# Optimization experiments

Measured on AMD Instinct MI355X. Metric: run time of the kernel, lower is better.

## Reference

```python
import jax, jax.numpy as jnp
import numpy as np

K = 512
H = 8

def setup_inputs() -> dict:
    key = jax.random.key(0)
    ks = jax.random.split(key, 6)
    b, t, k = 4, 2048, K
    scale = 1.0 / np.sqrt(k)
    return {
        "x": jax.random.normal(ks[0], (b, t, k), dtype=jnp.float32),
        "Wq": jax.random.normal(ks[1], (k, k), dtype=jnp.float32) * scale,
        "Wk": jax.random.normal(ks[2], (k, k), dtype=jnp.float32) * scale,
        "Wv": jax.random.normal(ks[3], (k, k), dtype=jnp.float32) * scale,
        "Wo": jax.random.normal(ks[4], (k, k), dtype=jnp.float32) * scale,
        "bo": jax.random.normal(ks[5], (k,), dtype=jnp.float32) * 0.01,
    }

def reference(x, Wq, Wk, Wv, Wo, bo):
    b, t, k = x.shape
    h = H
    s = k // h
    # nn.Linear: y = x @ W.T ; weights stored [out, in]
    q = (x @ Wq.T).reshape(b, t, h, s)
    kk = (x @ Wk.T).reshape(b, t, h, s)
    v = (x @ Wv.T).reshape(b, t, h, s)
    # scores: note original divides by sqrt(k) (full model dim), not sqrt(s)
    dot = jnp.einsum("bqhs,bkhs->bhqk", q, kk) / jnp.sqrt(jnp.float32(k))
    attn = jax.nn.softmax(dot, axis=-1)
    out = jnp.einsum("bhqk,bkhs->bqhs", attn, v).reshape(b, t, k)
    return out @ Wo.T + bo
```

## Files before the change

kernel.cpp:

```cpp
#include <hip/hip_runtime.h>

typedef _Float16 f16;
typedef _Float16 f16x8 __attribute__((ext_vector_type(8)));
typedef _Float16 f16x4 __attribute__((ext_vector_type(4)));
typedef float    f32x4 __attribute__((ext_vector_type(4)));
typedef __fp16   fp16x2 __attribute__((ext_vector_type(2)));

#define MFMA(a,b,c) __builtin_amdgcn_mfma_f32_16x16x32_f16((a),(b),(c),0,0,0)

#if __has_builtin(__builtin_amdgcn_exp2f)
#define EXP2(x) __builtin_amdgcn_exp2f(x)
#else
#define EXP2(x) exp2f(x)
#endif

__device__ __forceinline__ void gl_lds16(const void* g, void* l) {
  __builtin_amdgcn_global_load_lds(
      (__attribute__((address_space(1))) void*)(void*)(g),
      (__attribute__((address_space(3))) void*)(l),
      16, 0, 0);
}

__device__ __forceinline__ int SWZ(int row) {
  return ((row & 3) | ((row >> 1) & 4)) << 4;
}

__global__ __launch_bounds__(256) void k_convert(
    const float* __restrict__ x, const float* __restrict__ Wq,
    const float* __restrict__ Wk, const float* __restrict__ Wv,
    const float* __restrict__ Wo,
    f16* __restrict__ x_h, f16* __restrict__ wqkv_h, f16* __restrict__ wo_h) {
  const int XQ    = (8192 * 512) / 4;
  const int WQKVQ = (1536 * 512) / 4;
  const int WOQ   = (512 * 512) / 4;
  const int total = XQ + WQKVQ + WOQ;
  for (int q = blockIdx.x * blockDim.x + threadIdx.x; q < total;
       q += gridDim.x * blockDim.x) {
    const float* src;
    f16* dst;
    if (q < XQ) {
      src = x + q * 4;
      dst = x_h + q * 4;
    } else if (q < XQ + WQKVQ) {
      int j  = q - XQ;
      int r  = j >> 7;
      int c0 = (j & 127) * 4;
      const float* w = (r < 512) ? Wq : (r < 1024) ? Wk : Wv;
      src = w + (r & 511) * 512 + c0;
      dst = wqkv_h + j * 4;
    } else {
      int j = q - XQ - WQKVQ;
      src = Wo + j * 4;
      dst = wo_h + j * 4;
    }
    float4 v = *(const float4*)src;
    f16x4 o = {(f16)v.x, (f16)v.y, (f16)v.z, (f16)v.w};
    *(f16x4*)dst = o;
  }
}

__device__ __forceinline__ void gemm_core(const f16* __restrict__ A,
                                          const f16* __restrict__ B,
                                          int bm, int bn, f32x4 (&acc)[4][4],
                                          char* smem) {
  f16* As = (f16*)smem;
  f16* Bs = (f16*)(smem + 32768);
  const int tid  = threadIdx.x;
  const int lane = tid & 63;
  const int w    = tid >> 6;
  const int wr   = (w >> 1) & 1, wc = w & 1;
  const int r0   = tid >> 3;
  const int cb   = (tid & 7) << 4;

  auto stage = [&](int buf, int kt) {
#pragma unroll
    for (int inst = 0; inst < 4; ++inst) {
      const int row  = inst * 32 + r0;
      const int csrc = cb ^ ((row & 7) << 4);
      gl_lds16(A + (bm + row) * 512 + kt + (csrc >> 1),
               (char*)As + buf * 16384 + inst * 4096 + w * 1024);
      gl_lds16(B + (bn + row) * 512 + kt + (csrc >> 1),
               (char*)Bs + buf * 16384 + inst * 4096 + w * 1024);
    }
  };

  stage(0, 0);
#pragma unroll
  for (int t = 0; t < 8; ++t) {
    const int cur = t & 1;
    asm volatile("s_waitcnt vmcnt(0)" ::: "memory");
    __builtin_amdgcn_s_barrier();
    __builtin_amdgcn_sched_barrier(0);
    if (t < 7) stage(cur ^ 1, (t + 1) * 64);
    f16x8 af[4][2], bf[4][2];
#pragma unroll
    for (int i = 0; i < 4; ++i) {
      const int ra = wr * 64 + i * 16 + (lane & 15);
      const int rb = wc * 64 + i * 16 + (lane & 15);
#pragma unroll
      for (int ks = 0; ks < 2; ++ks) {
        const int cc = ks * 64 + ((lane >> 4) << 4);
        af[i][ks] = *(const f16x8*)((const char*)As + cur * 16384 + ra * 128 + (cc ^ ((ra & 7) << 4)));
        bf[i][ks] = *(const f16x8*)((const char*)Bs + cur * 16384 + rb * 128 + (cc ^ ((rb & 7) << 4)));
      }
    }
    __builtin_amdgcn_s_setprio(1);
#pragma unroll
    for (int i = 0; i < 4; ++i)
#pragma unroll
      for (int j = 0; j < 4; ++j) {
        acc[i][j] = MFMA(af[i][0], bf[j][0], acc[i][j]);
        acc[i][j] = MFMA(af[i][1], bf[j][1], acc[i][j]);
      }
    __builtin_amdgcn_s_setprio(0);
  }
}

__global__ __launch_bounds__(256) void k_gemm_qkv(
    const f16* __restrict__ A, const f16* __restrict__ B,
    f16* __restrict__ q_h, f16* __restrict__ k_h, f16* __restrict__ vt_h) {
  __shared__ char smem[65536];
  const int bm = blockIdx.x * 128;
  const int bn = blockIdx.y * 128;
  const bool isV = (bn >= 1024);

  f32x4 acc[4][4] = {};
  if (isV) gemm_core(B, A, bn, bm, acc, smem);
  else     gemm_core(A, B, bm, bn, acc, smem);

  const int tid  = threadIdx.x;
  const int lane = tid & 63;
  const int w    = tid >> 6;
  const int wr   = (w >> 1) & 1, wc = w & 1;
  const float qscale = (bn < 512) ? 0.044194173824159216f * 1.4426950408889634f : 1.0f;

  __syncthreads();
  f16* T = (f16*)smem;
#pragma unroll
  for (int i = 0; i < 4; ++i) {
    const int rr = wr * 64 + i * 16 + ((lane >> 4) << 2);
#pragma unroll
    for (int j = 0; j < 4; ++j) {
      const int cc = wc * 64 + j * 16 + (lane & 15);
#pragma unroll
      for (int r = 0; r < 4; ++r)
        T[(rr + r) * 136 + cc] = (f16)(acc[i][j][r] * qscale);
    }
  }
  __syncthreads();

  f16* dst_qk = (bn < 512) ? q_h : k_h;
#pragma unroll
  for (int k = 0; k < 8; ++k) {
    const int idx  = k * 256 + tid;
    const int row  = idx >> 4;
    const int col8 = (idx & 15) * 8;
    const f16x8 v = *(const f16x8*)(T + row * 136 + col8);
    if (!isV) {
      const int m = bm + row, b = m >> 11, t = m & 2047;
      const int nn = (bn + col8) & 511, h = nn >> 6, s = nn & 63;
      *(f16x8*)(dst_qk + ((size_t)((b * 8 + h) * 2048 + t)) * 64 + s) = v;
    } else {
      const int nn = (bn - 1024) + row, h = nn >> 6, s = nn & 63;
      const int m = bm + col8, b = m >> 11, t = m & 2047;
      *(f16x8*)(vt_h + ((size_t)((b * 8 + h) * 64 + s)) * 2048 + t) = v;
    }
  }
}

__global__ __launch_bounds__(512, 2) void k_attn(
    const f16* __restrict__ q_h, const f16* __restrict__ k_h,
    const f16* __restrict__ vt_h, f16* __restrict__ a_h) {
  __shared__ char smem[65536];

  const int tid  = threadIdx.x;
  const int lane = tid & 63;
  const int w    = tid >> 6;
  const int g    = w >> 2;
  const int wg   = w & 3;

  int id = blockIdx.x;
  id = (id & 7) * 32 + (id >> 3);
  const int qt = (id & 7) * 256;
  const int bh = id >> 3;

  const f16* qb = q_h + (size_t)bh * 2048 * 64;
  const f16* kb = k_h + (size_t)bh * 2048 * 64;
  const f16* vb = vt_h + (size_t)bh * 64 * 2048;

  auto KsP = [&](int grp, int buf) { return smem + grp * 32768 + buf * 16384; };
  auto VsP = [&](int grp, int buf) { return smem + grp * 32768 + buf * 16384 + 8192; };

  const int m  = lane & 15;
  const int hi = lane >> 4;

  f16x8 qf[4][2];
#pragma unroll
  for (int i = 0; i < 4; ++i) {
    const int qrow = qt + wg * 64 + i * 16 + m;
#pragma unroll
    for (int ks = 0; ks < 2; ++ks)
      qf[i][ks] = *(const f16x8*)(qb + qrow * 64 + ks * 32 + hi * 8);
  }

  f32x4 oacc[4][4] = {};
  float lsum[4]    = {0.f, 0.f, 0.f, 0.f};

  const int gt  = tid & 255;
  const int r0  = gt >> 3;
  const int cbb = (tid & 7) << 4;

  auto stage = [&](int buf, int t) {
    const int ktv = g * 1024 + t * 64;
#pragma unroll
    for (int inst = 0; inst < 2; ++inst) {
      const int row  = inst * 32 + r0;
      const int csrc = cbb ^ SWZ(row);
      gl_lds16(kb + (ktv + row) * 64 + (csrc >> 1),
               KsP(g, buf) + inst * 4096 + wg * 1024);
      gl_lds16(vb + row * 2048 + ktv + (csrc >> 1),
               VsP(g, buf) + inst * 4096 + wg * 1024);
    }
  };

  auto pack4 = [](float a, float b, float c, float d) -> unsigned long long {
    union { fp16x2 h2[2]; unsigned long long u; } t;
    t.h2[0] = __builtin_amdgcn_cvt_pkrtz(a, b);
    t.h2[1] = __builtin_amdgcn_cvt_pkrtz(c, d);
    return t.u;
  };

  auto tile = [&](const char* ksb, const char* vsb) {
    f16x8 kf[4][2];
#pragma unroll
    for (int n = 0; n < 4; ++n) {
      const int row = ((n >> 1) << 5) + ((m >> 2) << 3) + ((n & 1) << 2) + (m & 3);
      const int sw  = SWZ(row);
#pragma unroll
      for (int ks = 0; ks < 2; ++ks) {
        const int c = (ks * 64 + (hi << 4)) ^ sw;
        kf[n][ks] = *(const f16x8*)(ksb + row * 128 + c);
      }
    }
    f32x4 sf[4][4];
#pragma unroll
    for (int i = 0; i < 4; ++i)
#pragma unroll
      for (int n = 0; n < 4; ++n) {
        f32x4 s = {0.f, 0.f, 0.f, 0.f};
        s = MFMA(kf[n][0], qf[i][0], s);
        s = MFMA(kf[n][1], qf[i][1], s);
        sf[i][n] = s;
      }
    f16x8 pa[4][2];
#pragma unroll
    for (int i = 0; i < 4; ++i) {
      f32x4 e[4];
#pragma unroll
      for (int n = 0; n < 4; ++n) {
        e[n][0] = EXP2(sf[i][n][0]);
        e[n][1] = EXP2(sf[i][n][1]);
        e[n][2] = EXP2(sf[i][n][2]);
        e[n][3] = EXP2(sf[i][n][3]);
      }
      const f32x4 ssum = (e[0] + e[1]) + (e[2] + e[3]);
      lsum[i] += (ssum[0] + ssum[1]) + (ssum[2] + ssum[3]);
#pragma unroll
      for (int ks = 0; ks < 2; ++ks) {
        union { unsigned long long u[2]; f16x8 v; } u;
        u.u[0] = pack4(e[2 * ks][0], e[2 * ks][1], e[2 * ks][2], e[2 * ks][3]);
        u.u[1] = pack4(e[2 * ks + 1][0], e[2 * ks + 1][1],
                       e[2 * ks + 1][2], e[2 * ks + 1][3]);
        pa[i][ks] = u.v;
      }
    }
#pragma unroll
    for (int n = 0; n < 4; ++n) {
      const int row = n * 16 + m;
      const int sw  = SWZ(row);
      const f16x8 vf0 = *(const f16x8*)(vsb + row * 128 + ((hi << 4) ^ sw));
      const f16x8 vf1 = *(const f16x8*)(vsb + row * 128 + ((64 + (hi << 4)) ^ sw));
#pragma unroll
      for (int i = 0; i < 4; ++i) {
        oacc[i][n] = MFMA(pa[i][0], vf0, oacc[i][n]);
        oacc[i][n] = MFMA(pa[i][1], vf1, oacc[i][n]);
      }
    }
  };

  stage(0, 0);
  for (int j = 0; j < 16; ++j) {
    const int cur = j & 1;
    asm volatile("s_waitcnt vmcnt(0)" ::: "memory");
    __builtin_amdgcn_s_barrier();
    __builtin_amdgcn_sched_barrier(0);
    if (j < 15) stage(cur ^ 1, j + 1);
    tile(KsP(g, cur), VsP(g, cur));
  }

  float lfin[4];
#pragma unroll
  for (int i = 0; i < 4; ++i) {
    float t = lsum[i] + __shfl_xor(lsum[i], 16, 64);
    lfin[i] = t + __shfl_xor(t, 32, 64);
  }

  __syncthreads();
  float* Ol = (float*)smem;
  float* l1 = (float*)(smem + 34816);

  const int b2 = bh >> 3, h2 = bh & 7;
#pragma unroll
  for (int p = 0; p < 2; ++p) {
    if (g == 1 && (wg >> 1) == p) {
#pragma unroll
      for (int i = 0; i < 4; ++i)
#pragma unroll
        for (int r = 0; r < 4; ++r) {
          const int ql = (wg * 64 + i * 16 + hi * 4 + r) & 127;
#pragma unroll
          for (int n = 0; n < 4; ++n)
            Ol[ql * 68 + n * 16 + m] = oacc[i][n][r];
        }
      if (hi == 0)
#pragma unroll
        for (int i = 0; i < 4; ++i)
          l1[(wg * 64 + i * 16 + m) & 127] = lfin[i];
    }
    __syncthreads();
    if (g == 0 && (wg >> 1) == p) {
#pragma unroll
      for (int i = 0; i < 4; ++i) {
        float lself[4];
#pragma unroll
        for (int r = 0; r < 4; ++r)
          lself[r] = __shfl(lfin[i], (hi << 2) + r, 64);
#pragma unroll
        for (int r = 0; r < 4; ++r) {
          const int qg = wg * 64 + i * 16 + hi * 4 + r;
          const int ql = qg & 127;
          const float rl = 1.0f / (lself[r] + l1[ql]);
          const int qrow = qt + qg;
#pragma unroll
          for (int n = 0; n < 4; ++n) {
            const int s = n * 16 + m;
            const float o = oacc[i][n][r] + Ol[ql * 68 + s];
            a_h[(size_t)(b2 * 2048 + qrow) * 512 + h2 * 64 + s] = (f16)(o * rl);
          }
        }
      }
    }
    __syncthreads();
  }
}

__global__ __launch_bounds__(256) void k_gemm_out(
    const f16* __restrict__ A, const f16* __restrict__ B,
    const float* __restrict__ bo, float* __restrict__ out) {
  __shared__ char smem[65536];
  const int bm = blockIdx.x * 128;
  const int bn = blockIdx.y * 128;
  f32x4 acc[4][4] = {};
  gemm_core(A, B, bm, bn, acc, smem);

  const int tid  = threadIdx.x;
  const int lane = tid & 63;
  const int w    = tid >> 6;
  const int wr   = (w >> 1) & 1, wc = w & 1;
#pragma unroll
  for (int i = 0; i < 4; ++i) {
    const int m0 = bm + wr * 64 + i * 16 + ((lane >> 4) << 2);
#pragma unroll
    for (int j = 0; j < 4; ++j) {
      const int n = bn + wc * 64 + j * 16 + (lane & 15);
      const float bias = bo[n];
#pragma unroll
      for (int r = 0; r < 4; ++r)
        out[(size_t)(m0 + r) * 512 + n] = acc[i][j][r] + bias;
    }
  }
}

extern "C" void kernel_launch(void* const* d_in, const int* in_sizes, int n_in,
                              void* d_out, int out_size, void* d_ws, size_t ws_size,
                              hipStream_t stream) {
  const float* x  = (const float*)d_in[0];
  const float* Wq = (const float*)d_in[1];
  const float* Wk = (const float*)d_in[2];
  const float* Wv = (const float*)d_in[3];
  const float* Wo = (const float*)d_in[4];
  const float* bo = (const float*)d_in[5];
  float* out = (float*)d_out;

  char* ws = (char*)d_ws;
  f16* x_h    = (f16*)(ws);
  f16* wqkv_h = (f16*)(ws + 8388608);
  f16* wo_h   = (f16*)(ws + 9961472);
  f16* q_h    = (f16*)(ws + 10485760);
  f16* k_h    = (f16*)(ws + 18874368);
  f16* vt_h   = (f16*)(ws + 27262976);
  f16* a_h    = (f16*)(ws + 35651584);
  (void)ws_size; (void)in_sizes; (void)n_in; (void)out_size;

  k_convert<<<2048, 256, 0, stream>>>(x, Wq, Wk, Wv, Wo, x_h, wqkv_h, wo_h);
  k_gemm_qkv<<<dim3(64, 12), 256, 0, stream>>>(x_h, wqkv_h, q_h, k_h, vt_h);
  k_attn<<<256, 512, 0, stream>>>(q_h, k_h, vt_h, a_h);
  k_gemm_out<<<dim3(64, 4), 256, 0, stream>>>(a_h, wo_h, bo, out);
}
```

Before: 81.82 us.

## Fuse fp32-to-fp16 conversion of x into QKV GEMM loads and remap tiles

Removes the separate x conversion pass. The QKV GEMM now loads fp32 x tiles straight into registers, converts them to fp16 and writes them into swizzled LDS, while weight tiles still go through direct global-to-LDS loads. This saves a full write and re-read of the 8 MB fp16 copy of x. The grid becomes 1D with a tile remapping that groups blocks, likely to improve L2 reuse across XCDs. The cost is register pressure and VALU conversion work inside the GEMM, and every N-tile block that shares the same x rows now converts them again.

```diff
diff --git a/kernel.cpp b/kernel.cpp
--- a/kernel.cpp
+++ b/kernel.cpp
@@ -25,31 +25,25 @@
   return ((row & 3) | ((row >> 1) & 4)) << 4;
 }
 
-__global__ __launch_bounds__(256) void k_convert(
-    const float* __restrict__ x, const float* __restrict__ Wq,
-    const float* __restrict__ Wk, const float* __restrict__ Wv,
-    const float* __restrict__ Wo,
-    f16* __restrict__ x_h, f16* __restrict__ wqkv_h, f16* __restrict__ wo_h) {
-  const int XQ    = (8192 * 512) / 4;
+__global__ __launch_bounds__(256) void k_convert_w(
+    const float* __restrict__ Wq, const float* __restrict__ Wk,
+    const float* __restrict__ Wv, const float* __restrict__ Wo,
+    f16* __restrict__ wqkv_h, f16* __restrict__ wo_h) {
   const int WQKVQ = (1536 * 512) / 4;
   const int WOQ   = (512 * 512) / 4;
-  const int total = XQ + WQKVQ + WOQ;
+  const int total = WQKVQ + WOQ;
   for (int q = blockIdx.x * blockDim.x + threadIdx.x; q < total;
        q += gridDim.x * blockDim.x) {
     const float* src;
     f16* dst;
-    if (q < XQ) {
-      src = x + q * 4;
-      dst = x_h + q * 4;
-    } else if (q < XQ + WQKVQ) {
-      int j  = q - XQ;
-      int r  = j >> 7;
-      int c0 = (j & 127) * 4;
+    if (q < WQKVQ) {
+      int r  = q >> 7;
+      int c0 = (q & 127) * 4;
       const float* w = (r < 512) ? Wq : (r < 1024) ? Wk : Wv;
       src = w + (r & 511) * 512 + c0;
-      dst = wqkv_h + j * 4;
+      dst = wqkv_h + q * 4;
     } else {
-      int j = q - XQ - WQKVQ;
+      int j = q - WQKVQ;
       src = Wo + j * 4;
       dst = wo_h + j * 4;
     }
@@ -116,17 +110,102 @@
   }
 }
 
+template <bool XA>
+__device__ __forceinline__ void gemm_core_fx(const float* __restrict__ X, int bx,
+                                             const f16* __restrict__ W, int bw,
+                                             f32x4 (&acc)[4][4], char* smem) {
+  char* XsB = smem + (XA ? 0 : 32768);
+  char* WsB = smem + (XA ? 32768 : 0);
+  const int tid  = threadIdx.x;
+  const int lane = tid & 63;
+  const int w    = tid >> 6;
+  const int wr   = (w >> 1) & 1, wc = w & 1;
+  const int r0   = tid >> 3;
+  const int cb   = (tid & 7) << 4;
+
+  float4 xr[4][2];
+  auto loadX = [&](int kt) {
+#pragma unroll
+    for (int inst = 0; inst < 4; ++inst) {
+      const int row  = inst * 32 + r0;
+      const int csrc = cb ^ ((row & 7) << 4);
+      const float* src = X + (size_t)(bx + row) * 512 + kt + (csrc >> 1);
+      xr[inst][0] = *(const float4*)src;
+      xr[inst][1] = *(const float4*)(src + 4);
+    }
+  };
+  auto writeX = [&](int buf) {
+#pragma unroll
+    for (int inst = 0; inst < 4; ++inst) {
+      f16x8 h;
+      h[0] = (f16)xr[inst][0].x; h[1] = (f16)xr[inst][0].y;
+      h[2] = (f16)xr[inst][0].z; h[3] = (f16)xr[inst][0].w;
+      h[4] = (f16)xr[inst][1].x; h[5] = (f16)xr[inst][1].y;
+      h[6] = (f16)xr[inst][1].z; h[7] = (f16)xr[inst][1].w;
+      *(f16x8*)(XsB + buf * 16384 + inst * 4096 + tid * 16) = h;
+    }
+  };
+  auto stageW = [&](int buf, int kt) {
+#pragma unroll
+    for (int inst = 0; inst < 4; ++inst) {
+      const int row  = inst * 32 + r0;
+      const int csrc = cb ^ ((row & 7) << 4);
+      gl_lds16(W + (bw + row) * 512 + kt + (csrc >> 1),
+               WsB + buf * 16384 + inst * 4096 + w * 1024);
+    }
+  };
+
+  loadX(0);
+  stageW(0, 0);
+  writeX(0);
+#pragma unroll
+  for (int t = 0; t < 8; ++t) {
+    const int cur = t & 1;
+    asm volatile("s_waitcnt vmcnt(0) lgkmcnt(0)" ::: "memory");
+    __builtin_amdgcn_s_barrier();
+    __builtin_amdgcn_sched_barrier(0);
+    if (t < 7) {
+      loadX((t + 1) * 64);
+      stageW(cur ^ 1, (t + 1) * 64);
+    }
+    f16x8 af[4][2], bf[4][2];
+#pragma unroll
+    for (int i = 0; i < 4; ++i) {
+      const int ra = wr * 64 + i * 16 + (lane & 15);
+      const int rb = wc * 64 + i * 16 + (lane & 15);
+#pragma unroll
+      for (int ks = 0; ks < 2; ++ks) {
+        const int cc = ks * 64 + ((lane >> 4) << 4);
+        af[i][ks] = *(const f16x8*)(smem + cur * 16384 + ra * 128 + (cc ^ ((ra & 7) << 4)));
+        bf[i][ks] = *(const f16x8*)(smem + 32768 + cur * 16384 + rb * 128 + (cc ^ ((rb & 7) << 4)));
+      }
+    }
+    __builtin_amdgcn_s_setprio(1);
+#pragma unroll
+    for (int i = 0; i < 4; ++i)
+#pragma unroll
+      for (int j = 0; j < 4; ++j) {
+        acc[i][j] = MFMA(af[i][0], bf[j][0], acc[i][j]);
+        acc[i][j] = MFMA(af[i][1], bf[j][1], acc[i][j]);
+      }
+    __builtin_amdgcn_s_setprio(0);
+    if (t < 7) writeX(cur ^ 1);
+  }
+}
+
 __global__ __launch_bounds__(256) void k_gemm_qkv(
-    const f16* __restrict__ A, const f16* __restrict__ B,
+    const float* __restrict__ X, const f16* __restrict__ B,
     f16* __restrict__ q_h, f16* __restrict__ k_h, f16* __restrict__ vt_h) {
   __shared__ char smem[65536];
-  const int bm = blockIdx.x * 128;
-  const int bn = blockIdx.y * 128;
+  int wg = blockIdx.x;
+  const int nw  = (wg & 7) * 96 + (wg >> 3);
+  const int bm  = (nw / 12) * 128;
+  const int bn  = (nw % 12) * 128;
   const bool isV = (bn >= 1024);
 
   f32x4 acc[4][4] = {};
-  if (isV) gemm_core(B, A, bn, bm, acc, smem);
-  else     gemm_core(A, B, bm, bn, acc, smem);
+  if (isV) gemm_core_fx<false>(X, bm, B, bn, acc, smem);
+  else     gemm_core_fx<true>(X, bm, B, bn, acc, smem);
 
   const int tid  = threadIdx.x;
   const int lane = tid & 63;
@@ -393,7 +472,6 @@
   float* out = (float*)d_out;
 
   char* ws = (char*)d_ws;
-  f16* x_h    = (f16*)(ws);
   f16* wqkv_h = (f16*)(ws + 8388608);
   f16* wo_h   = (f16*)(ws + 9961472);
   f16* q_h    = (f16*)(ws + 10485760);
@@ -402,8 +480,8 @@
   f16* a_h    = (f16*)(ws + 35651584);
   (void)ws_size; (void)in_sizes; (void)n_in; (void)out_size;
 
-  k_convert<<<2048, 256, 0, stream>>>(x, Wq, Wk, Wv, Wo, x_h, wqkv_h, wo_h);
-  k_gemm_qkv<<<dim3(64, 12), 256, 0, stream>>>(x_h, wqkv_h, q_h, k_h, vt_h);
+  k_convert_w<<<512, 256, 0, stream>>>(Wq, Wk, Wv, Wo, wqkv_h, wo_h);
+  k_gemm_qkv<<<768, 256, 0, stream>>>(x, wqkv_h, q_h, k_h, vt_h);
   k_attn<<<256, 512, 0, stream>>>(q_h, k_h, vt_h, a_h);
   k_gemm_out<<<dim3(64, 4), 256, 0, stream>>>(a_h, wo_h, bo, out);
 }
```

Result: slower. 84.00 us (+2.7%).
